# Optimization experiments

Hardware: AMD Instinct MI355X
Metric: run time of the kernel (lower is better)

The kernel has to match this reference:

```python
import jax, jax.numpy as jnp
import numpy as np

N, C, S, NS = 65536, 64, 8, 16  # points, channels, share_planes, nsample
CS = C // S
EPS = 1e-5


def _bn(x, g, b, m, v):
    # BatchNorm1d in eval mode over the last (channel) axis
    return (x - m) * (g * jax.lax.rsqrt(v + EPS)) + b


def setup_inputs() -> dict:
    key = jax.random.key(0)
    ks = jax.random.split(key, 32)
    rn = lambda k, s: jax.random.normal(k, s, jnp.float32)
    un = lambda k, s: jax.random.uniform(k, s, jnp.float32, 0.5, 1.5)
    return {
        "p": rn(ks[0], (N, 3)),
        "x": rn(ks[1], (N, C)),
        "idx": jax.random.randint(ks[2], (N, NS), 0, N),
        "Wq": rn(ks[3], (C, C)) * 0.1, "bq": rn(ks[4], (C,)) * 0.1,
        "Wk": rn(ks[5], (C, C)) * 0.1, "bk": rn(ks[6], (C,)) * 0.1,
        "Wv": rn(ks[7], (C, C)) * 0.1, "bv": rn(ks[8], (C,)) * 0.1,
        "Wp1": rn(ks[9], (3, 3)) * 0.3, "bp1": rn(ks[10], (3,)) * 0.1,
        "pg": un(ks[11], (3,)), "pb": rn(ks[12], (3,)) * 0.1,
        "pm": rn(ks[13], (3,)) * 0.1, "pv": un(ks[14], (3,)),
        "Wp2": rn(ks[15], (C, 3)) * 0.3, "bp2": rn(ks[16], (C,)) * 0.1,
        "wg1": un(ks[17], (C,)), "wb1": rn(ks[18], (C,)) * 0.1,
        "wm1": rn(ks[19], (C,)) * 0.1, "wv1": un(ks[20], (C,)),
        "Ww1": rn(ks[21], (CS, C)) * 0.1, "bw1": rn(ks[22], (CS,)) * 0.1,
        "wg2": un(ks[23], (CS,)), "wb2": rn(ks[24], (CS,)) * 0.1,
        "wm2": rn(ks[25], (CS,)) * 0.1, "wv2": un(ks[26], (CS,)),
        "Ww2": rn(ks[27], (CS, CS)) * 0.1, "bw2": rn(ks[28], (CS,)) * 0.1,
    }


def _forward(p, x, idx, Wq, bq, Wk, bk, Wv, bv, Wp1, bp1, pg, pb, pm, pv,
             Wp2, bp2, wg1, wb1, wm1, wv1, Ww1, bw1, wg2, wb2, wm2, wv2, Ww2, bw2):
    xq = x @ Wq.T + bq                      # [N, C]
    xk = (x @ Wk.T + bk)[idx]               # [N, NS, C] neighbor gather
    xv = (x @ Wv.T + bv)[idx]               # [N, NS, C]
    pr = p[idx] - p[:, None, :]             # [N, NS, 3] relative coords (queryandgroup use_xyz)
    # linear_p: Conv1d(3,3,1) -> BN(3) -> ReLU -> Conv1d(3,C,1) (pointwise)
    t = jax.nn.relu(_bn(pr @ Wp1.T + bp1, pg, pb, pm, pv))
    pr = t @ Wp2.T + bp2                    # [N, NS, C] positional encoding
    # out_planes // mid_planes == 1, so p_r.view(...).sum(2) is identity
    w = xk - xq[:, None, :] + pr            # [N, NS, C] relation
    # linear_w: BN(C) -> ReLU -> Conv(C,C/S) -> BN(C/S) -> ReLU -> Conv(C/S,C/S)
    w = jax.nn.relu(_bn(w, wg1, wb1, wm1, wv1))
    w = jax.nn.relu(_bn(w @ Ww1.T + bw1, wg2, wb2, wm2, wv2))
    w = w @ Ww2.T + bw2                     # [N, NS, C//S]
    w = jax.nn.softmax(w, axis=1)           # softmax over the neighbor axis
    out = ((xv + pr).reshape(N, NS, S, CS) * w[:, :, None, :]).sum(axis=1)
    return out.reshape(N, C)


def reference(p, x, idx, Wq, bq, Wk, bk, Wv, bv, Wp1, bp1, pg, pb, pm, pv,
              Wp2, bp2, wg1, wb1, wm1, wv1, Ww1, bw1, wg2, wb2, wm2, wv2, Ww2, bw2):
    return _forward(p, x, idx, Wq, bq, Wk, bk, Wv, bv, Wp1, bp1, pg, pb, pm, pv,
                    Wp2, bp2, wg1, wb1, wm1, wv1, Ww1, bw1, wg2, wb2, wm2, wv2, Ww2, bw2)
```

## Files before the change

kernel.cpp:

```cpp
#include <hip/hip_runtime.h>

#define NPTS 65536
#define EPSV 1e-5f

typedef unsigned int uint_t;
typedef unsigned short ushort_t;
typedef __attribute__((ext_vector_type(8))) short short8;
typedef __attribute__((ext_vector_type(4))) float float4v;

union U8 { uint4 u; short8 s; };

__device__ __forceinline__ ushort_t f2bf(float f) {
    unsigned u = __float_as_uint(f);
    unsigned r = (u + 0x7fffu + ((u >> 16) & 1u)) >> 16;
    return (ushort_t)r;
}

__device__ __forceinline__ uint_t pkrn(uint_t lo, uint_t hi) {
    return ((lo + 0x8000u) >> 16) | ((hi + 0x8000u) & 0xffff0000u);
}

__device__ __forceinline__ short8 packA(const float* p8) {
    uint4 a = *(const uint4*)p8;
    uint4 b = *(const uint4*)(p8 + 4);
    U8 c;
    c.u.x = pkrn(a.x, a.y); c.u.y = pkrn(a.z, a.w);
    c.u.z = pkrn(b.x, b.y); c.u.w = pkrn(b.z, b.w);
    return c.s;
}

__device__ __forceinline__ short8 packG(const float* p8) {
    float4 a = *(const float4*)p8;
    float4 b = *(const float4*)(p8 + 4);
    U8 c;
    c.u.x = pkrn(__float_as_uint(a.x), __float_as_uint(a.y));
    c.u.y = pkrn(__float_as_uint(a.z), __float_as_uint(a.w));
    c.u.z = pkrn(__float_as_uint(b.x), __float_as_uint(b.y));
    c.u.w = pkrn(__float_as_uint(b.z), __float_as_uint(b.w));
    return c.s;
}

#define WBAR() do { asm volatile("s_waitcnt lgkmcnt(0)" ::: "memory"); \
                    __builtin_amdgcn_wave_barrier(); } while (0)

__global__ __launch_bounds__(256) void k_qkv(
    const float* __restrict__ x,
    const float* __restrict__ Wq, const float* __restrict__ bq,
    const float* __restrict__ Wk, const float* __restrict__ bk,
    const float* __restrict__ Wv, const float* __restrict__ bv,
    float* __restrict__ xq, uint_t* __restrict__ kvp)
{
    __shared__ __align__(16) ushort_t sA[64 * 72];
    __shared__ __align__(16) ushort_t sB[192 * 72];

    const int tid  = threadIdx.x;
    const int lane = tid & 63;
    const int w    = tid >> 6;
    const int n0   = blockIdx.x * 64;

    const float4* xg = (const float4*)(x + (size_t)n0 * 64);
#pragma unroll
    for (int i = 0; i < 4; ++i) {
        int f = i * 256 + tid;
        float4 v = xg[f];
        int r = f >> 4, c4 = f & 15;
        uint2 pk;
        pk.x = (uint_t)f2bf(v.x) | ((uint_t)f2bf(v.y) << 16);
        pk.y = (uint_t)f2bf(v.z) | ((uint_t)f2bf(v.w) << 16);
        *(uint2*)(sA + r * 72 + c4 * 4) = pk;
    }
#pragma unroll
    for (int i = 0; i < 12; ++i) {
        const float* src = (i < 4) ? Wq : (i < 8) ? Wk : Wv;
        int f = i * 256 + tid;
        int r = f >> 4, c4 = f & 15;
        float4 v = ((const float4*)src)[(i & 3) * 256 + tid];
        uint2 pk;
        pk.x = (uint_t)f2bf(v.x) | ((uint_t)f2bf(v.y) << 16);
        pk.y = (uint_t)f2bf(v.z) | ((uint_t)f2bf(v.w) << 16);
        *(uint2*)(sB + r * 72 + c4 * 4) = pk;
    }
    __syncthreads();

    const int quad = lane >> 4;
    const int cn   = lane & 15;
    const int mrow = (w << 4) + cn;

    short8 a0 = *(const short8*)(sA + mrow * 72 + quad * 8);
    short8 a1 = *(const short8*)(sA + mrow * 72 + 32 + quad * 8);

    float4v acc[12];
#pragma unroll
    for (int t = 0; t < 12; ++t) {
        const int brow = t * 16 + cn;
        short8 b0 = *(const short8*)(sB + brow * 72 + quad * 8);
        short8 b1 = *(const short8*)(sB + brow * 72 + 32 + quad * 8);
        float4v c = {0.f, 0.f, 0.f, 0.f};
        c = __builtin_amdgcn_mfma_f32_16x16x32_bf16(a0, b0, c, 0, 0, 0);
        c = __builtin_amdgcn_mfma_f32_16x16x32_bf16(a1, b1, c, 0, 0, 0);
        acc[t] = c;
    }

    const int orow = n0 + (w << 4) + quad * 4;
#pragma unroll
    for (int t = 0; t < 4; ++t) {
        int o = t * 16 + cn;
        float bqv = bq[o], bkv = bk[o], bvv = bv[o];
        float4v aq = acc[t], ak = acc[4 + t], av = acc[8 + t];
#pragma unroll
        for (int r = 0; r < 4; ++r) {
            size_t base = (size_t)(orow + r) * 64 + o;
            xq[base]  = aq[r] + bqv;
            kvp[base] = (uint_t)f2bf(ak[r] + bkv) | ((uint_t)f2bf(av[r] + bvv) << 16);
        }
    }
}

__global__ __launch_bounds__(256, 3) void k_attn(
    const float* __restrict__ p, const int* __restrict__ idx,
    const float* __restrict__ xq, const uint_t* __restrict__ kvp,
    const float* __restrict__ Wp1, const float* __restrict__ bp1,
    const float* __restrict__ pg, const float* __restrict__ pb,
    const float* __restrict__ pm, const float* __restrict__ pv,
    const float* __restrict__ Wp2, const float* __restrict__ bp2,
    const float* __restrict__ wg1, const float* __restrict__ wb1,
    const float* __restrict__ wm1, const float* __restrict__ wv1,
    const float* __restrict__ Ww1, const float* __restrict__ bw1,
    const float* __restrict__ wg2, const float* __restrict__ wb2,
    const float* __restrict__ wm2, const float* __restrict__ wv2,
    const float* __restrict__ Ww2, const float* __restrict__ bw2,
    float* __restrict__ out)
{
    __shared__ __align__(16) float sw[4][16 * 68];
    __shared__ __align__(16) float shl[4][16 * 36];
    __shared__ float swg[4][16 * 9 + 4];

    const int tid   = threadIdx.x;
    const int wid   = __builtin_amdgcn_readfirstlane(tid >> 6);
    const int lane  = tid & 63;
    const int nbase = blockIdx.x * 16 + wid * 4;

    float* wrel = sw[wid];
    float* hL   = shl[wid];
    float* wgt  = swg[wid];

    const int cm  = lane & 15;
    const int q   = lane >> 4;
    const int m8  = lane & 7;
    const int cmc = cm & 7;
    const bool colv = cm < 8;

    const int* idxr = idx + (size_t)nbase * 16;

    uint_t ga[16], gb[16];
    auto issueF = [&](int pt, uint_t (&dst)[16]) {
#pragma unroll
        for (int j = 0; j < 16; ++j) {
            int id = __builtin_amdgcn_readfirstlane(idxr[pt * 16 + j]);
            dst[j] = kvp[(size_t)id * 64 + lane];
        }
    };

    issueF(0, ga);
    issueF(1, gb);

    for (int i = lane; i < 16 * 36; i += 64) hL[i] = 0.f;

    int   idv[4];
    float xqc[4];
#pragma unroll
    for (int pt = 0; pt < 4; ++pt) {
        idv[pt] = idxr[pt * 16 + cm];
        xqc[pt] = xq[(size_t)(nbase + pt) * 64 + lane];
    }
    float gpx[4], gpy[4], gpz[4];
#pragma unroll
    for (int pt = 0; pt < 4; ++pt) {
        gpx[pt] = p[idv[pt] * 3 + 0];
        gpy[pt] = p[idv[pt] * 3 + 1];
        gpz[pt] = p[idv[pt] * 3 + 2];
    }

    float w100 = Wp1[0], w101 = Wp1[1], w102 = Wp1[2];
    float w110 = Wp1[3], w111 = Wp1[4], w112 = Wp1[5];
    float w120 = Wp1[6], w121 = Wp1[7], w122 = Wp1[8];
    float sp0 = pg[0] * rsqrtf(pv[0] + EPSV);
    float sp1 = pg[1] * rsqrtf(pv[1] + EPSV);
    float sp2 = pg[2] * rsqrtf(pv[2] + EPSV);
    float off0 = (bp1[0] - pm[0]) * sp0 + pb[0];
    float off1 = (bp1[1] - pm[1]) * sp1 + pb[1];
    float off2 = (bp1[2] - pm[2]) * sp2 + pb[2];

    float s1 = wg1[lane] * rsqrtf(wv1[lane] + EPSV);
    float o1 = wb1[lane] - wm1[lane] * s1;
    float wp2x = Wp2[lane * 3 + 0], wp2y = Wp2[lane * 3 + 1], wp2z = Wp2[lane * 3 + 2];
    float peb = bp2[lane];

    float s2c = wg2[cmc] * rsqrtf(wv2[cmc] + EPSV);
    float o2c = wb2[cmc] - wm2[cmc] * s2c;
    float bw1c = bw1[cmc];

    short8 bf1a, bf1b, bf2;
    {
        const float* r1 = Ww1 + cmc * 64 + q * 8;
        short8 t1a = packG(r1);
        short8 t1b = packG(r1 + 32);
        short8 t2  = packG(Ww2 + cmc * 8);
        U8 z; z.u = make_uint4(0u, 0u, 0u, 0u);
        bf1a = colv ? t1a : z.s;
        bf1b = colv ? t1b : z.s;
        bf2  = (colv && q == 0) ? t2 : z.s;
    }

    float t0a[4], t1a[4], t2a[4];
#pragma unroll
    for (int pt = 0; pt < 4; ++pt) {
        int n = nbase + pt;
        float pcx = p[n * 3 + 0], pcy = p[n * 3 + 1], pcz = p[n * 3 + 2];
        float prx = gpx[pt] - pcx, pry = gpy[pt] - pcy, prz = gpz[pt] - pcz;
        t0a[pt] = fmaxf(fmaf(fmaf(prx, w100, fmaf(pry, w101, prz * w102)), sp0, off0), 0.f);
        t1a[pt] = fmaxf(fmaf(fmaf(prx, w110, fmaf(pry, w111, prz * w112)), sp1, off1), 0.f);
        t2a[pt] = fmaxf(fmaf(fmaf(prx, w120, fmaf(pry, w121, prz * w122)), sp2, off2), 0.f);
    }

    auto computeF = [&](int pt, uint_t (&g)[16]) {
        float t0v = t0a[pt], t1v = t1a[pt], t2v = t2a[pt];
        float xqv = xqc[pt];
        float vpe[16];
#pragma unroll
        for (int j = 0; j < 16; ++j) {
            float tt0 = __uint_as_float(__builtin_amdgcn_readlane(__float_as_uint(t0v), j));
            float tt1 = __uint_as_float(__builtin_amdgcn_readlane(__float_as_uint(t1v), j));
            float tt2 = __uint_as_float(__builtin_amdgcn_readlane(__float_as_uint(t2v), j));
            float pe = fmaf(tt0, wp2x, fmaf(tt1, wp2y, fmaf(tt2, wp2z, peb)));
            float xkj = __uint_as_float(g[j] << 16);
            float xvj = __uint_as_float(g[j] & 0xffff0000u);
            vpe[j] = xvj + pe;
            wrel[j * 68 + lane] = fmaxf(fmaf(xkj - xqv + pe, s1, o1), 0.f);
        }
        WBAR();

        short8 a1a = packA(wrel + cm * 68 + q * 8);
        short8 a1b = packA(wrel + cm * 68 + 32 + q * 8);
        float4v d1 = {0.f, 0.f, 0.f, 0.f};
        d1 = __builtin_amdgcn_mfma_f32_16x16x32_bf16(a1a, bf1a, d1, 0, 0, 0);
        d1 = __builtin_amdgcn_mfma_f32_16x16x32_bf16(a1b, bf1b, d1, 0, 0, 0);
#pragma unroll
        for (int r = 0; r < 4; ++r) {
            float hv = fmaxf(fmaf(d1[r] + bw1c, s2c, o2c), 0.f);
            if (colv) hL[(q * 4 + r) * 36 + cm] = hv;
        }
        WBAR();

        short8 a2 = packA(hL + cm * 36 + q * 8);
        float4v d2 = {0.f, 0.f, 0.f, 0.f};
        d2 = __builtin_amdgcn_mfma_f32_16x16x32_bf16(a2, bf2, d2, 0, 0, 0);

        float mx = fmaxf(fmaxf(d2[0], d2[1]), fmaxf(d2[2], d2[3]));
        mx = fmaxf(mx, __shfl_xor(mx, 16));
        mx = fmaxf(mx, __shfl_xor(mx, 32));
        float e0 = __expf(d2[0] - mx), e1 = __expf(d2[1] - mx);
        float e2 = __expf(d2[2] - mx), e3 = __expf(d2[3] - mx);
        float ss = e0 + e1 + e2 + e3;
        ss += __shfl_xor(ss, 16);
        ss += __shfl_xor(ss, 32);
        float inv = 1.f / ss;
        if (colv) {
            wgt[(q * 4 + 0) * 9 + cm] = e0 * inv;
            wgt[(q * 4 + 1) * 9 + cm] = e1 * inv;
            wgt[(q * 4 + 2) * 9 + cm] = e2 * inv;
            wgt[(q * 4 + 3) * 9 + cm] = e3 * inv;
        }
        WBAR();

        float acc = 0.f;
#pragma unroll
        for (int j = 0; j < 16; ++j) acc = fmaf(wgt[j * 9 + m8], vpe[j], acc);
        WBAR();
        out[(size_t)(nbase + pt) * 64 + lane] = acc;
    };

    computeF(0, ga);
    issueF(2, ga);
    computeF(1, gb);
    issueF(3, gb);
    computeF(2, ga);
    computeF(3, gb);
}

extern "C" void kernel_launch(void* const* d_in, const int* in_sizes, int n_in,
                              void* d_out, int out_size, void* d_ws, size_t ws_size,
                              hipStream_t stream) {
    const float* p   = (const float*)d_in[0];
    const float* x   = (const float*)d_in[1];
    const int*   idx = (const int*)d_in[2];
    const float* Wq  = (const float*)d_in[3];  const float* bq  = (const float*)d_in[4];
    const float* Wk  = (const float*)d_in[5];  const float* bk  = (const float*)d_in[6];
    const float* Wv  = (const float*)d_in[7];  const float* bv  = (const float*)d_in[8];
    const float* Wp1 = (const float*)d_in[9];  const float* bp1 = (const float*)d_in[10];
    const float* pg  = (const float*)d_in[11]; const float* pb  = (const float*)d_in[12];
    const float* pm  = (const float*)d_in[13]; const float* pv  = (const float*)d_in[14];
    const float* Wp2 = (const float*)d_in[15]; const float* bp2 = (const float*)d_in[16];
    const float* wg1 = (const float*)d_in[17]; const float* wb1 = (const float*)d_in[18];
    const float* wm1 = (const float*)d_in[19]; const float* wv1 = (const float*)d_in[20];
    const float* Ww1 = (const float*)d_in[21]; const float* bw1 = (const float*)d_in[22];
    const float* wg2 = (const float*)d_in[23]; const float* wb2 = (const float*)d_in[24];
    const float* wm2 = (const float*)d_in[25]; const float* wv2 = (const float*)d_in[26];
    const float* Ww2 = (const float*)d_in[27]; const float* bw2 = (const float*)d_in[28];

    float*  xqw = (float*)d_ws;
    uint_t* kvw = (uint_t*)((char*)d_ws + (size_t)NPTS * 64 * sizeof(float));
    float*  outp = (float*)d_out;

    k_qkv<<<dim3(NPTS / 64), dim3(256), 0, stream>>>(x, Wq, bq, Wk, bk, Wv, bv, xqw, kvw);
    k_attn<<<dim3(NPTS / 16), dim3(256), 0, stream>>>(p, idx, xqw, kvw,
                                                      Wp1, bp1, pg, pb, pm, pv, Wp2, bp2,
                                                      wg1, wb1, wm1, wv1, Ww1, bw1,
                                                      wg2, wb2, wm2, wv2, Ww2, bw2, outp);
}
```

Before: 190.4 us.

## Stage attention intermediates as bf16 in LDS and vectorize weight/position reads

The relation tile and the hidden activations are now written to LDS as bf16 instead of fp32, so the MFMA A operands load directly as short8 without repacking. The per-point position MLP features are stored once to LDS as float4 and read back, replacing three readlane broadcasts per neighbour. The softmax weights are stored and read as float4 rows. Occupancy in launch bounds goes from 3 to 4 blocks per CU, cutting LDS use and the register budget per thread, which risks spills. Rounding to bf16 now happens on store rather than in packA, so the numerics are unchanged.

```diff
diff --git a/kernel.cpp b/kernel.cpp
--- a/kernel.cpp
+++ b/kernel.cpp
@@ -18,15 +18,6 @@
 
 __device__ __forceinline__ uint_t pkrn(uint_t lo, uint_t hi) {
     return ((lo + 0x8000u) >> 16) | ((hi + 0x8000u) & 0xffff0000u);
-}
-
-__device__ __forceinline__ short8 packA(const float* p8) {
-    uint4 a = *(const uint4*)p8;
-    uint4 b = *(const uint4*)(p8 + 4);
-    U8 c;
-    c.u.x = pkrn(a.x, a.y); c.u.y = pkrn(a.z, a.w);
-    c.u.z = pkrn(b.x, b.y); c.u.w = pkrn(b.z, b.w);
-    return c.s;
 }
 
 __device__ __forceinline__ short8 packG(const float* p8) {
@@ -116,7 +107,7 @@
     }
 }
 
-__global__ __launch_bounds__(256, 3) void k_attn(
+__global__ __launch_bounds__(256, 4) void k_attn(
     const float* __restrict__ p, const int* __restrict__ idx,
     const float* __restrict__ xq, const uint_t* __restrict__ kvp,
     const float* __restrict__ Wp1, const float* __restrict__ bp1,
@@ -131,18 +122,20 @@
     const float* __restrict__ Ww2, const float* __restrict__ bw2,
     float* __restrict__ out)
 {
-    __shared__ __align__(16) float sw[4][16 * 68];
-    __shared__ __align__(16) float shl[4][16 * 36];
-    __shared__ float swg[4][16 * 9 + 4];
+    __shared__ __align__(16) ushort_t swr[4][16 * 72];
+    __shared__ __align__(16) ushort_t shl[4][16 * 40];
+    __shared__ __align__(16) float    swt[4][4 * 16 * 4];
+    __shared__ __align__(16) float    swg[4][8 * 20];
 
     const int tid   = threadIdx.x;
     const int wid   = __builtin_amdgcn_readfirstlane(tid >> 6);
     const int lane  = tid & 63;
     const int nbase = blockIdx.x * 16 + wid * 4;
 
-    float* wrel = sw[wid];
-    float* hL   = shl[wid];
-    float* wgt  = swg[wid];
+    ushort_t* wrelh = swr[wid];
+    ushort_t* hLh   = shl[wid];
+    float*    stt   = swt[wid];
+    float*    wgt   = swg[wid];
 
     const int cm  = lane & 15;
     const int q   = lane >> 4;
@@ -164,7 +157,10 @@
     issueF(0, ga);
     issueF(1, gb);
 
-    for (int i = lane; i < 16 * 36; i += 64) hL[i] = 0.f;
+    {
+        uint_t* hz = (uint_t*)hLh;
+        for (int i = lane; i < 16 * 20; i += 64) hz[i] = 0u;
+    }
 
     int   idv[4];
     float xqc[4];
@@ -212,47 +208,49 @@
         bf2  = (colv && q == 0) ? t2 : z.s;
     }
 
-    float t0a[4], t1a[4], t2a[4];
 #pragma unroll
     for (int pt = 0; pt < 4; ++pt) {
         int n = nbase + pt;
         float pcx = p[n * 3 + 0], pcy = p[n * 3 + 1], pcz = p[n * 3 + 2];
         float prx = gpx[pt] - pcx, pry = gpy[pt] - pcy, prz = gpz[pt] - pcz;
-        t0a[pt] = fmaxf(fmaf(fmaf(prx, w100, fmaf(pry, w101, prz * w102)), sp0, off0), 0.f);
-        t1a[pt] = fmaxf(fmaf(fmaf(prx, w110, fmaf(pry, w111, prz * w112)), sp1, off1), 0.f);
-        t2a[pt] = fmaxf(fmaf(fmaf(prx, w120, fmaf(pry, w121, prz * w122)), sp2, off2), 0.f);
-    }
+        float t0 = fmaxf(fmaf(fmaf(prx, w100, fmaf(pry, w101, prz * w102)), sp0, off0), 0.f);
+        float t1 = fmaxf(fmaf(fmaf(prx, w110, fmaf(pry, w111, prz * w112)), sp1, off1), 0.f);
+        float t2 = fmaxf(fmaf(fmaf(prx, w120, fmaf(pry, w121, prz * w122)), sp2, off2), 0.f);
+        if (lane < 16) {
+            float4 tv = make_float4(t0, t1, t2, 0.f);
+            *(float4*)(stt + (pt * 16 + cm) * 4) = tv;
+        }
+    }
+    WBAR();
 
     auto computeF = [&](int pt, uint_t (&g)[16]) {
-        float t0v = t0a[pt], t1v = t1a[pt], t2v = t2a[pt];
         float xqv = xqc[pt];
         float vpe[16];
 #pragma unroll
         for (int j = 0; j < 16; ++j) {
-            float tt0 = __uint_as_float(__builtin_amdgcn_readlane(__float_as_uint(t0v), j));
-            float tt1 = __uint_as_float(__builtin_amdgcn_readlane(__float_as_uint(t1v), j));
-            float tt2 = __uint_as_float(__builtin_amdgcn_readlane(__float_as_uint(t2v), j));
-            float pe = fmaf(tt0, wp2x, fmaf(tt1, wp2y, fmaf(tt2, wp2z, peb)));
+            float4 t = *(const float4*)(stt + (pt * 16 + j) * 4);
+            float pe = fmaf(t.x, wp2x, fmaf(t.y, wp2y, fmaf(t.z, wp2z, peb)));
             float xkj = __uint_as_float(g[j] << 16);
             float xvj = __uint_as_float(g[j] & 0xffff0000u);
             vpe[j] = xvj + pe;
-            wrel[j * 68 + lane] = fmaxf(fmaf(xkj - xqv + pe, s1, o1), 0.f);
+            float d = (xkj - xqv) + pe;
+            wrelh[j * 72 + lane] = f2bf(fmaxf(fmaf(d, s1, o1), 0.f));
         }
         WBAR();
 
-        short8 a1a = packA(wrel + cm * 68 + q * 8);
-        short8 a1b = packA(wrel + cm * 68 + 32 + q * 8);
+        short8 a1a = *(const short8*)(wrelh + cm * 72 + q * 8);
+        short8 a1b = *(const short8*)(wrelh + cm * 72 + 32 + q * 8);
         float4v d1 = {0.f, 0.f, 0.f, 0.f};
         d1 = __builtin_amdgcn_mfma_f32_16x16x32_bf16(a1a, bf1a, d1, 0, 0, 0);
         d1 = __builtin_amdgcn_mfma_f32_16x16x32_bf16(a1b, bf1b, d1, 0, 0, 0);
 #pragma unroll
         for (int r = 0; r < 4; ++r) {
             float hv = fmaxf(fmaf(d1[r] + bw1c, s2c, o2c), 0.f);
-            if (colv) hL[(q * 4 + r) * 36 + cm] = hv;
+            if (colv) hLh[(q * 4 + r) * 40 + cm] = f2bf(hv);
         }
         WBAR();
 
-        short8 a2 = packA(hL + cm * 36 + q * 8);
+        short8 a2 = *(const short8*)(hLh + cm * 40 + q * 8);
         float4v d2 = {0.f, 0.f, 0.f, 0.f};
         d2 = __builtin_amdgcn_mfma_f32_16x16x32_bf16(a2, bf2, d2, 0, 0, 0);
 
@@ -266,16 +264,20 @@
         ss += __shfl_xor(ss, 32);
         float inv = 1.f / ss;
         if (colv) {
-            wgt[(q * 4 + 0) * 9 + cm] = e0 * inv;
-            wgt[(q * 4 + 1) * 9 + cm] = e1 * inv;
-            wgt[(q * 4 + 2) * 9 + cm] = e2 * inv;
-            wgt[(q * 4 + 3) * 9 + cm] = e3 * inv;
+            float4 wv4 = make_float4(e0 * inv, e1 * inv, e2 * inv, e3 * inv);
+            *(float4*)(wgt + cm * 20 + q * 4) = wv4;
         }
         WBAR();
 
         float acc = 0.f;
 #pragma unroll
-        for (int j = 0; j < 16; ++j) acc = fmaf(wgt[j * 9 + m8], vpe[j], acc);
+        for (int gq = 0; gq < 4; ++gq) {
+            float4 wv4 = *(const float4*)(wgt + m8 * 20 + gq * 4);
+            acc = fmaf(wv4.x, vpe[gq * 4 + 0], acc);
+            acc = fmaf(wv4.y, vpe[gq * 4 + 1], acc);
+            acc = fmaf(wv4.z, vpe[gq * 4 + 2], acc);
+            acc = fmaf(wv4.w, vpe[gq * 4 + 3], acc);
+        }
         WBAR();
         out[(size_t)(nbase + pt) * 64 + lane] = acc;
     };
```

Result: faster. 184.7 us (-3.0%).
